# Kernel optimization log

Hardware: AMD Instinct MI355X
Metric: run time of the kernel (lower is better)

## Reference

```python
import jax, jax.numpy as jnp
import numpy as np

N_NODES = 100000
N_EDGES = 1600000
IN_DIM, FEAT_DIM, HID_DIM, OUT_DIM = 128, 64, 64, 64


def _linear_params(key, fan_in, fan_out):
    kw, kb = jax.random.split(key)
    bound = 1.0 / np.sqrt(fan_in)
    W = jax.random.uniform(kw, (fan_out, fan_in), jnp.float32, -bound, bound)
    b = jax.random.uniform(kb, (fan_out,), jnp.float32, -bound, bound)
    return W, b


def setup_inputs() -> dict:
    key = jax.random.key(0)
    k_x, k1, k2, k3, k_e = jax.random.split(key, 5)
    x = jax.random.normal(k_x, (N_NODES, IN_DIM), jnp.float32)
    edge_index = jax.random.randint(k_e, (2, N_EDGES), 0, N_NODES, jnp.int32)
    W_pre, b_pre = _linear_params(k1, IN_DIM, FEAT_DIM)
    W_first, b_first = _linear_params(k2, FEAT_DIM, HID_DIM)
    W_out, b_out = _linear_params(k3, HID_DIM, OUT_DIM)
    return {"x": x, "edge_index": edge_index,
            "W_pre": W_pre, "b_pre": b_pre,
            "W_first": W_first, "b_first": b_first,
            "W_out": W_out, "b_out": b_out}


def _gin_conv(x, src, dst, W, b):
    # out_i = nn((1+eps)*x_i + sum_{j: (j->i)} x_j), eps=0 (PyG GINConv default)
    msgs = x[src]                                   # [E, d] gather
    agg = jax.ops.segment_sum(msgs, dst, num_segments=x.shape[0])  # [N, d]
    return (x + agg) @ W.T + b


def reference(x, edge_index, W_pre, b_pre, W_first, b_first, W_out, b_out):
    src, dst = edge_index[0], edge_index[1]
    h = x @ W_pre.T + b_pre                         # feature_pre linear
    h = _gin_conv(h, src, dst, W_first, b_first)
    h = jax.nn.relu(h)                              # dropout: eval mode no-op
    h = _gin_conv(h, src, dst, W_out, b_out)
    return h
```

## Files before the change

kernel.cpp:

```cpp
#include <hip/hip_runtime.h>


using bf16x8 = __attribute__((ext_vector_type(8))) short;
using f32x4  = __attribute__((ext_vector_type(4))) float;

__device__ inline unsigned short f2bf(float f) {
    unsigned b = __float_as_uint(f);
    return (unsigned short)((b + 0x7FFF + ((b >> 16) & 1)) >> 16);
}
__device__ inline float bf2f_lo(unsigned u) { return __uint_as_float(u << 16); }
__device__ inline float bf2f_hi(unsigned u) { return __uint_as_float(u & 0xFFFF0000u); }
__device__ inline unsigned packbf(float lo, float hi) {
    return (unsigned)f2bf(lo) | ((unsigned)f2bf(hi) << 16);
}
__device__ inline void acc8(float* a, const uint4 u) {
    a[0] += bf2f_lo(u.x); a[1] += bf2f_hi(u.x);
    a[2] += bf2f_lo(u.y); a[3] += bf2f_hi(u.y);
    a[4] += bf2f_lo(u.z); a[5] += bf2f_hi(u.z);
    a[6] += bf2f_lo(u.w); a[7] += bf2f_hi(u.w);
}

constexpr int CHUNK = 4096;
constexpr int LCAP  = 1024;

__global__ __launch_bounds__(256) void k1_pre_hist(
    const float* __restrict__ x, const float* __restrict__ Wp,
    const float* __restrict__ bp, unsigned short* __restrict__ h16a, int N,
    const int* __restrict__ dst, int* __restrict__ ccounts,
    int E, int NBKC, int NC, int GB)
{
    __shared__ char lds_raw[34816];
    const int tid = threadIdx.x;

    if (blockIdx.x >= GB) {
        int* cnt = (int*)lds_raw;
        const int c = blockIdx.x - GB;
        for (int b = tid; b < NBKC; b += 256) cnt[b] = 0;
        __syncthreads();
        const int beg = c * CHUNK, end = min(beg + CHUNK, E);
        for (int e = beg + tid; e < end; e += 256)
            atomicAdd(&cnt[dst[e] >> 8], 1);
        __syncthreads();
        for (int b = tid; b < NBKC; b += 256) ccounts[b * NC + c] = cnt[b];
        return;
    }

    constexpr int SP = 136;
    unsigned short (*xs)[SP] = (unsigned short(*)[SP])lds_raw;
    unsigned short (*ws)[SP] = (unsigned short(*)[SP])(lds_raw + 64 * SP * 2);
    const int base = blockIdx.x * 64;

    for (int i = tid; i < 64 * 32; i += 256) {
        const int r = i >> 5, q = i & 31;
        const float4 v = *(const float4*)(Wp + r * 128 + q * 4);
        *(ushort4*)&ws[r][q * 4] =
            make_ushort4(f2bf(v.x), f2bf(v.y), f2bf(v.z), f2bf(v.w));
    }
    for (int i = tid; i < 64 * 32; i += 256) {
        const int r = i >> 5, q = i & 31;
        int row = base + r; if (row > N - 1) row = N - 1;
        const float4 v = *(const float4*)(x + (size_t)row * 128 + q * 4);
        *(ushort4*)&xs[r][q * 4] =
            make_ushort4(f2bf(v.x), f2bf(v.y), f2bf(v.z), f2bf(v.w));
    }
    __syncthreads();

    const int w = tid >> 6, l = tid & 63, lr = l & 15, lg = l >> 4;
    f32x4 acc[4];
#pragma unroll
    for (int nb = 0; nb < 4; ++nb) {
        const float bv = bp[nb * 16 + lr];
        acc[nb] = (f32x4){bv, bv, bv, bv};
    }
#pragma unroll
    for (int kb = 0; kb < 4; ++kb) {
        const bf16x8 a = *(const bf16x8*)&xs[w * 16 + lr][kb * 32 + lg * 8];
#pragma unroll
        for (int nb = 0; nb < 4; ++nb) {
            const bf16x8 b = *(const bf16x8*)&ws[nb * 16 + lr][kb * 32 + lg * 8];
            acc[nb] = __builtin_amdgcn_mfma_f32_16x16x32_bf16(a, b, acc[nb], 0, 0, 0);
        }
    }
#pragma unroll
    for (int nb = 0; nb < 4; ++nb) {
#pragma unroll
        for (int r = 0; r < 4; ++r) {
            const int row = base + w * 16 + lg * 4 + r;
            if (row < N)
                h16a[(size_t)row * 64 + nb * 16 + lr] = f2bf(acc[nb][r]);
        }
    }
}

__global__ __launch_bounds__(512) void k_blocksum(
    const int* __restrict__ in, int* __restrict__ partial, int n)
{
    __shared__ int s[512];
    const int i = blockIdx.x * 512 + threadIdx.x;
    s[threadIdx.x] = (i < n) ? in[i] : 0;
    __syncthreads();
    for (int off = 256; off > 0; off >>= 1) {
        if (threadIdx.x < off) s[threadIdx.x] += s[threadIdx.x + off];
        __syncthreads();
    }
    if (threadIdx.x == 0) partial[blockIdx.x] = s[0];
}

__global__ __launch_bounds__(1024) void k_scanpartial1024(
    int* __restrict__ partial, int nblk)
{
    __shared__ int s[1024];
    const int t = threadIdx.x;
    s[t] = (t < nblk) ? partial[t] : 0;
    __syncthreads();
    for (int off = 1; off < 1024; off <<= 1) {
        const int v = (t >= off) ? s[t - off] : 0;
        __syncthreads();
        s[t] += v;
        __syncthreads();
    }
    if (t < nblk) partial[t] = (t == 0) ? 0 : s[t - 1];
}

__global__ __launch_bounds__(512) void k_exscan(
    int* __restrict__ data, const int* __restrict__ partial, int n)
{
    __shared__ int s[512];
    const int i = blockIdx.x * 512 + threadIdx.x;
    const int t = threadIdx.x;
    const int v = (i < n) ? data[i] : 0;
    s[t] = v;
    __syncthreads();
    for (int off = 1; off < 512; off <<= 1) {
        const int u = (t >= off) ? s[t - off] : 0;
        __syncthreads();
        s[t] += u;
        __syncthreads();
    }
    if (i < n) data[i] = partial[blockIdx.x] + s[t] - v;
}

__global__ __launch_bounds__(256) void p_coarse(
    const int* __restrict__ src, const int* __restrict__ dst,
    const int* __restrict__ ccounts, unsigned* __restrict__ slots,
    int E, int NBKC, int NC)
{
    __shared__ int cur[512];
    const int c = blockIdx.x;
    for (int b = threadIdx.x; b < NBKC; b += 256) cur[b] = ccounts[b * NC + c];
    __syncthreads();
    const int beg = c * CHUNK;
    const int end = min(beg + CHUNK, E);
    for (int e = beg + threadIdx.x; e < end; e += 256) {
        const int d = dst[e];
        const int pos = atomicAdd(&cur[d >> 8], 1);
        slots[pos] = ((unsigned)(d & 255) << 24) | (unsigned)src[e];
    }
}

__global__ __launch_bounds__(256) void p_fine(
    const unsigned* __restrict__ slots, const int* __restrict__ ccounts,
    unsigned* __restrict__ slots2, int* __restrict__ noffs,
    int E, int N, int NBKC, int NC)
{
    __shared__ int hist[256], psum[256], cur[256];
    const int cb  = blockIdx.x;
    const int tid = threadIdx.x;
    const int cbase = ccounts[cb * NC];
    const int cend  = (cb + 1 < NBKC) ? ccounts[(cb + 1) * NC] : E;

    hist[tid] = 0;
    __syncthreads();
    for (int i = cbase + tid; i < cend; i += 256)
        atomicAdd(&hist[slots[i] >> 24], 1);
    __syncthreads();

    psum[tid] = hist[tid];
    __syncthreads();
    for (int off = 1; off < 256; off <<= 1) {
        const int v = (tid >= off) ? psum[tid - off] : 0;
        __syncthreads();
        psum[tid] += v;
        __syncthreads();
    }
    const int o = cbase + psum[tid] - hist[tid];
    cur[tid] = o;
    const int gnode = cb * 256 + tid;
    if (gnode < N) noffs[gnode] = o;
    if (cb == NBKC - 1 && tid == 0) noffs[N] = cend;
    __syncthreads();

    for (int i = cbase + tid; i < cend; i += 256) {
        const unsigned p = slots[i];
        const int pos = atomicAdd(&cur[p >> 24], 1);
        slots2[pos] = p & 0x00FFFFFFu;
    }
}

template <int RELU, int WF32>
__global__ __launch_bounds__(128) void conv_fused(
    const unsigned short* __restrict__ hin, const unsigned* __restrict__ slots2,
    const int* __restrict__ noffs, const float* __restrict__ W,
    const float* __restrict__ bias, float* __restrict__ outf,
    unsigned short* __restrict__ out16, int N)
{
    constexpr int SPW = 72;
    __shared__ unsigned short ws[64][SPW];
    __shared__ unsigned short xs[32][SPW];
    __shared__ unsigned lsl[LCAP];
    __shared__ int loffs[33];
    __shared__ int steal;

    const int tid  = threadIdx.x;
    const int base = blockIdx.x * 32;

    for (int i = tid; i < 64 * 16; i += 128) {
        const int r = i >> 4, q = i & 15;
        const float4 v = *(const float4*)(W + r * 64 + q * 4);
        *(ushort4*)&ws[r][q * 4] =
            make_ushort4(f2bf(v.x), f2bf(v.y), f2bf(v.z), f2bf(v.w));
    }
    if (tid <= 32) loffs[tid] = noffs[min(base + tid, N)];
    if (tid == 0) steal = 0;
    __syncthreads();

    const int beg = loffs[0];
    const int cnt = loffs[32] - beg;
    for (int i = tid; i < min(cnt, LCAP); i += 128) lsl[i] = slots2[beg + i];
    __syncthreads();

    const int l = tid & 63;
    const int leader = l & ~7;
    const int c = (l & 7) * 8;
    while (true) {
        int n = 0;
        if ((l & 7) == 0) n = atomicAdd(&steal, 1);
        n = __shfl(n, leader);
        if (n >= 32) break;
        const int node = base + n;
        float a[8] = {0.f, 0.f, 0.f, 0.f, 0.f, 0.f, 0.f, 0.f};
        if (node < N) {
            acc8(a, *(const uint4*)(hin + (size_t)node * 64 + c));
            int j = loffs[n] - beg;
            const int hi = loffs[n + 1] - beg;
            const int hiL = min(hi, LCAP);
            for (; j + 8 <= hiL; j += 8) {
                const unsigned s0 = lsl[j],     s1 = lsl[j + 1];
                const unsigned s2 = lsl[j + 2], s3 = lsl[j + 3];
                const unsigned s4 = lsl[j + 4], s5 = lsl[j + 5];
                const unsigned s6 = lsl[j + 6], s7 = lsl[j + 7];
                const uint4 u0 = *(const uint4*)(hin + (size_t)s0 * 64 + c);
                const uint4 u1 = *(const uint4*)(hin + (size_t)s1 * 64 + c);
                const uint4 u2 = *(const uint4*)(hin + (size_t)s2 * 64 + c);
                const uint4 u3 = *(const uint4*)(hin + (size_t)s3 * 64 + c);
                const uint4 u4 = *(const uint4*)(hin + (size_t)s4 * 64 + c);
                const uint4 u5 = *(const uint4*)(hin + (size_t)s5 * 64 + c);
                const uint4 u6 = *(const uint4*)(hin + (size_t)s6 * 64 + c);
                const uint4 u7 = *(const uint4*)(hin + (size_t)s7 * 64 + c);
                acc8(a, u0); acc8(a, u1); acc8(a, u2); acc8(a, u3);
                acc8(a, u4); acc8(a, u5); acc8(a, u6); acc8(a, u7);
            }
            for (; j + 4 <= hiL; j += 4) {
                const unsigned s0 = lsl[j],     s1 = lsl[j + 1];
                const unsigned s2 = lsl[j + 2], s3 = lsl[j + 3];
                const uint4 u0 = *(const uint4*)(hin + (size_t)s0 * 64 + c);
                const uint4 u1 = *(const uint4*)(hin + (size_t)s1 * 64 + c);
                const uint4 u2 = *(const uint4*)(hin + (size_t)s2 * 64 + c);
                const uint4 u3 = *(const uint4*)(hin + (size_t)s3 * 64 + c);
                acc8(a, u0); acc8(a, u1); acc8(a, u2); acc8(a, u3);
            }
            for (; j < hiL; ++j)
                acc8(a, *(const uint4*)(hin + (size_t)lsl[j] * 64 + c));
            for (; j < hi; ++j) {
                const unsigned s = slots2[beg + j];
                acc8(a, *(const uint4*)(hin + (size_t)s * 64 + c));
            }
        }
        *(uint4*)&xs[n][c] =
            make_uint4(packbf(a[0], a[1]), packbf(a[2], a[3]),
                       packbf(a[4], a[5]), packbf(a[6], a[7]));
    }
    __syncthreads();

    const int w = tid >> 6, lr = l & 15, lg = l >> 4;
    f32x4 acc[4];
#pragma unroll
    for (int nb = 0; nb < 4; ++nb) {
        const float bv = bias[nb * 16 + lr];
        acc[nb] = (f32x4){bv, bv, bv, bv};
    }
#pragma unroll
    for (int kb = 0; kb < 2; ++kb) {
        const bf16x8 a = *(const bf16x8*)&xs[w * 16 + lr][kb * 32 + lg * 8];
#pragma unroll
        for (int nb = 0; nb < 4; ++nb) {
            const bf16x8 b = *(const bf16x8*)&ws[nb * 16 + lr][kb * 32 + lg * 8];
            acc[nb] = __builtin_amdgcn_mfma_f32_16x16x32_bf16(a, b, acc[nb], 0, 0, 0);
        }
    }
#pragma unroll
    for (int nb = 0; nb < 4; ++nb) {
#pragma unroll
        for (int r = 0; r < 4; ++r) {
            const int row = base + w * 16 + lg * 4 + r;
            if (row < N) {
                float v = acc[nb][r];
                if (RELU) v = fmaxf(v, 0.f);
                if (WF32) outf[(size_t)row * 64 + nb * 16 + lr] = v;
                else      out16[(size_t)row * 64 + nb * 16 + lr] = f2bf(v);
            }
        }
    }
}

extern "C" void kernel_launch(void* const* d_in, const int* in_sizes, int n_in,
                              void* d_out, int out_size, void* d_ws, size_t ws_size,
                              hipStream_t stream)
{
    const float* x       = (const float*)d_in[0];
    const int*   ei      = (const int*)  d_in[1];
    const float* W_pre   = (const float*)d_in[2];
    const float* b_pre   = (const float*)d_in[3];
    const float* W_first = (const float*)d_in[4];
    const float* b_first = (const float*)d_in[5];
    const float* W_out   = (const float*)d_in[6];
    const float* b_out   = (const float*)d_in[7];

    const int N = in_sizes[0] / 128;
    const int E = in_sizes[1] / 2;
    const int* src = ei;
    const int* dst = ei + E;

    const int NBKC  = (N + 255) / 256;
    const int NC    = (E + CHUNK - 1) / CHUNK;
    const int nscan = NBKC * NC;
    const int nsblk = (nscan + 511) / 512;
    const int GB    = (N + 63) / 64;
    const int CB    = (N + 31) / 32;

    unsigned short* h16a   = (unsigned short*)d_ws;
    unsigned short* h16b   = h16a + (size_t)N * 64;
    unsigned*       slots  = (unsigned*)(h16b + (size_t)N * 64);
    unsigned*       slots2 = slots + E;
    int*            ccounts= (int*)(slots2 + E);
    int*            partial= ccounts + nscan;
    int*            noffs  = partial + 1024;

    float* out = (float*)d_out;

    k1_pre_hist<<<GB + NC, 256, 0, stream>>>(
        x, W_pre, b_pre, h16a, N, dst, ccounts, E, NBKC, NC, GB);

    k_blocksum<<<nsblk, 512, 0, stream>>>(ccounts, partial, nscan);
    k_scanpartial1024<<<1, 1024, 0, stream>>>(partial, nsblk);
    k_exscan<<<nsblk, 512, 0, stream>>>(ccounts, partial, nscan);

    p_coarse<<<NC, 256, 0, stream>>>(src, dst, ccounts, slots, E, NBKC, NC);
    p_fine<<<NBKC, 256, 0, stream>>>(slots, ccounts, slots2, noffs, E, N, NBKC, NC);

    conv_fused<1, 0><<<CB, 128, 0, stream>>>(
        h16a, slots2, noffs, W_first, b_first, nullptr, h16b, N);

    conv_fused<0, 1><<<CB, 128, 0, stream>>>(
        h16b, slots2, noffs, W_out, b_out, out, nullptr, N);
}
```

Measured before the change: 139.4 us.

## Split pre-GEMM across coarse/fine partition kernels and load W fragments into registers

Moves the input linear layer tiles out of the histogram kernel and splits them in half, running each half as extra blocks of the coarse-scatter and fine-sort kernels. This fills the small, latency-bound partition launches with independent compute work. The conv kernel also drops its LDS weight staging and loads the bf16 weight fragments straight from global memory into registers, reading noffs directly. The cost is more register pressure and larger LDS use in the sort kernels, which share a binary with the GEMM path.

```diff
diff --git a/kernel.cpp b/kernel.cpp
--- a/kernel.cpp
+++ b/kernel.cpp
@@ -23,32 +23,14 @@
 constexpr int CHUNK = 4096;
 constexpr int LCAP  = 1024;
 
-__global__ __launch_bounds__(256) void k1_pre_hist(
-    const float* __restrict__ x, const float* __restrict__ Wp,
-    const float* __restrict__ bp, unsigned short* __restrict__ h16a, int N,
-    const int* __restrict__ dst, int* __restrict__ ccounts,
-    int E, int NBKC, int NC, int GB)
-{
-    __shared__ char lds_raw[34816];
+__device__ __forceinline__ void pre_gemm_tile(
+    int base, const float* __restrict__ x, const float* __restrict__ Wp,
+    const float* __restrict__ bp, unsigned short* __restrict__ h16a, int N)
+{
+    constexpr int SP = 136;
+    __shared__ unsigned short xs[64][SP];
+    __shared__ unsigned short ws[64][SP];
     const int tid = threadIdx.x;
-
-    if (blockIdx.x >= GB) {
-        int* cnt = (int*)lds_raw;
-        const int c = blockIdx.x - GB;
-        for (int b = tid; b < NBKC; b += 256) cnt[b] = 0;
-        __syncthreads();
-        const int beg = c * CHUNK, end = min(beg + CHUNK, E);
-        for (int e = beg + tid; e < end; e += 256)
-            atomicAdd(&cnt[dst[e] >> 8], 1);
-        __syncthreads();
-        for (int b = tid; b < NBKC; b += 256) ccounts[b * NC + c] = cnt[b];
-        return;
-    }
-
-    constexpr int SP = 136;
-    unsigned short (*xs)[SP] = (unsigned short(*)[SP])lds_raw;
-    unsigned short (*ws)[SP] = (unsigned short(*)[SP])(lds_raw + 64 * SP * 2);
-    const int base = blockIdx.x * 64;
 
     for (int i = tid; i < 64 * 32; i += 256) {
         const int r = i >> 5, q = i & 31;
@@ -92,6 +74,22 @@
     }
 }
 
+__global__ __launch_bounds__(256) void p_hist(
+    const int* __restrict__ dst, int* __restrict__ ccounts,
+    int E, int NBKC, int NC)
+{
+    __shared__ int cnt[512];
+    const int tid = threadIdx.x;
+    const int c = blockIdx.x;
+    for (int b = tid; b < NBKC; b += 256) cnt[b] = 0;
+    __syncthreads();
+    const int beg = c * CHUNK, end = min(beg + CHUNK, E);
+    for (int e = beg + tid; e < end; e += 256)
+        atomicAdd(&cnt[dst[e] >> 8], 1);
+    __syncthreads();
+    for (int b = tid; b < NBKC; b += 256) ccounts[b * NC + c] = cnt[b];
+}
+
 __global__ __launch_bounds__(512) void k_blocksum(
     const int* __restrict__ in, int* __restrict__ partial, int n)
 {
@@ -140,61 +138,73 @@
     if (i < n) data[i] = partial[blockIdx.x] + s[t] - v;
 }
 
-__global__ __launch_bounds__(256) void p_coarse(
+__global__ __launch_bounds__(256) void k_coarse_gemm(
     const int* __restrict__ src, const int* __restrict__ dst,
     const int* __restrict__ ccounts, unsigned* __restrict__ slots,
-    int E, int NBKC, int NC)
-{
-    __shared__ int cur[512];
-    const int c = blockIdx.x;
-    for (int b = threadIdx.x; b < NBKC; b += 256) cur[b] = ccounts[b * NC + c];
-    __syncthreads();
-    const int beg = c * CHUNK;
-    const int end = min(beg + CHUNK, E);
-    for (int e = beg + threadIdx.x; e < end; e += 256) {
-        const int d = dst[e];
-        const int pos = atomicAdd(&cur[d >> 8], 1);
-        slots[pos] = ((unsigned)(d & 255) << 24) | (unsigned)src[e];
-    }
-}
-
-__global__ __launch_bounds__(256) void p_fine(
+    const float* __restrict__ x, const float* __restrict__ Wp,
+    const float* __restrict__ bp, unsigned short* __restrict__ h16a,
+    int N, int E, int NBKC, int NC)
+{
+    if ((int)blockIdx.x < NC) {
+        __shared__ int cur[512];
+        const int c = blockIdx.x;
+        for (int b = threadIdx.x; b < NBKC; b += 256) cur[b] = ccounts[b * NC + c];
+        __syncthreads();
+        const int beg = c * CHUNK;
+        const int end = min(beg + CHUNK, E);
+        for (int e = beg + threadIdx.x; e < end; e += 256) {
+            const int d = dst[e];
+            const int pos = atomicAdd(&cur[d >> 8], 1);
+            slots[pos] = ((unsigned)(d & 255) << 24) | (unsigned)src[e];
+        }
+        return;
+    }
+    pre_gemm_tile((blockIdx.x - NC) * 64, x, Wp, bp, h16a, N);
+}
+
+__global__ __launch_bounds__(256) void k_fine_gemm(
     const unsigned* __restrict__ slots, const int* __restrict__ ccounts,
     unsigned* __restrict__ slots2, int* __restrict__ noffs,
-    int E, int N, int NBKC, int NC)
-{
-    __shared__ int hist[256], psum[256], cur[256];
-    const int cb  = blockIdx.x;
-    const int tid = threadIdx.x;
-    const int cbase = ccounts[cb * NC];
-    const int cend  = (cb + 1 < NBKC) ? ccounts[(cb + 1) * NC] : E;
-
-    hist[tid] = 0;
-    __syncthreads();
-    for (int i = cbase + tid; i < cend; i += 256)
-        atomicAdd(&hist[slots[i] >> 24], 1);
-    __syncthreads();
-
-    psum[tid] = hist[tid];
-    __syncthreads();
-    for (int off = 1; off < 256; off <<= 1) {
-        const int v = (tid >= off) ? psum[tid - off] : 0;
-        __syncthreads();
-        psum[tid] += v;
-        __syncthreads();
-    }
-    const int o = cbase + psum[tid] - hist[tid];
-    cur[tid] = o;
-    const int gnode = cb * 256 + tid;
-    if (gnode < N) noffs[gnode] = o;
-    if (cb == NBKC - 1 && tid == 0) noffs[N] = cend;
-    __syncthreads();
-
-    for (int i = cbase + tid; i < cend; i += 256) {
-        const unsigned p = slots[i];
-        const int pos = atomicAdd(&cur[p >> 24], 1);
-        slots2[pos] = p & 0x00FFFFFFu;
-    }
+    const float* __restrict__ x, const float* __restrict__ Wp,
+    const float* __restrict__ bp, unsigned short* __restrict__ h16a,
+    int GA, int N, int E, int NBKC, int NC)
+{
+    if ((int)blockIdx.x < NBKC) {
+        __shared__ int hist[256], psum[256], cur[256];
+        const int cb  = blockIdx.x;
+        const int tid = threadIdx.x;
+        const int cbase = ccounts[cb * NC];
+        const int cend  = (cb + 1 < NBKC) ? ccounts[(cb + 1) * NC] : E;
+
+        hist[tid] = 0;
+        __syncthreads();
+        for (int i = cbase + tid; i < cend; i += 256)
+            atomicAdd(&hist[slots[i] >> 24], 1);
+        __syncthreads();
+
+        psum[tid] = hist[tid];
+        __syncthreads();
+        for (int off = 1; off < 256; off <<= 1) {
+            const int v = (tid >= off) ? psum[tid - off] : 0;
+            __syncthreads();
+            psum[tid] += v;
+            __syncthreads();
+        }
+        const int o = cbase + psum[tid] - hist[tid];
+        cur[tid] = o;
+        const int gnode = cb * 256 + tid;
+        if (gnode < N) noffs[gnode] = o;
+        if (cb == NBKC - 1 && tid == 0) noffs[N] = cend;
+        __syncthreads();
+
+        for (int i = cbase + tid; i < cend; i += 256) {
+            const unsigned p = slots[i];
+            const int pos = atomicAdd(&cur[p >> 24], 1);
+            slots2[pos] = p & 0x00FFFFFFu;
+        }
+        return;
+    }
+    pre_gemm_tile((GA + blockIdx.x - NBKC) * 64, x, Wp, bp, h16a, N);
 }
 
 template <int RELU, int WF32>
@@ -205,7 +215,6 @@
     unsigned short* __restrict__ out16, int N)
 {
     constexpr int SPW = 72;
-    __shared__ unsigned short ws[64][SPW];
     __shared__ unsigned short xs[32][SPW];
     __shared__ unsigned lsl[LCAP];
     __shared__ int loffs[33];
@@ -214,18 +223,11 @@
     const int tid  = threadIdx.x;
     const int base = blockIdx.x * 32;
 
-    for (int i = tid; i < 64 * 16; i += 128) {
-        const int r = i >> 4, q = i & 15;
-        const float4 v = *(const float4*)(W + r * 64 + q * 4);
-        *(ushort4*)&ws[r][q * 4] =
-            make_ushort4(f2bf(v.x), f2bf(v.y), f2bf(v.z), f2bf(v.w));
-    }
     if (tid <= 32) loffs[tid] = noffs[min(base + tid, N)];
     if (tid == 0) steal = 0;
-    __syncthreads();
-
-    const int beg = loffs[0];
-    const int cnt = loffs[32] - beg;
+    const int beg  = noffs[base];
+    const int cend = noffs[min(base + 32, N)];
+    const int cnt  = cend - beg;
     for (int i = tid; i < min(cnt, LCAP); i += 128) lsl[i] = slots2[beg + i];
     __syncthreads();
 
@@ -283,6 +285,23 @@
     __syncthreads();
 
     const int w = tid >> 6, lr = l & 15, lg = l >> 4;
+    bf16x8 wf[2][4];
+#pragma unroll
+    for (int kb = 0; kb < 2; ++kb) {
+#pragma unroll
+        for (int nb = 0; nb < 4; ++nb) {
+            const float* wp = W + (nb * 16 + lr) * 64 + kb * 32 + lg * 8;
+            const float4 v0 = *(const float4*)wp;
+            const float4 v1 = *(const float4*)(wp + 4);
+            bf16x8 b;
+            b[0] = (short)f2bf(v0.x); b[1] = (short)f2bf(v0.y);
+            b[2] = (short)f2bf(v0.z); b[3] = (short)f2bf(v0.w);
+            b[4] = (short)f2bf(v1.x); b[5] = (short)f2bf(v1.y);
+            b[6] = (short)f2bf(v1.z); b[7] = (short)f2bf(v1.w);
+            wf[kb][nb] = b;
+        }
+    }
+
     f32x4 acc[4];
 #pragma unroll
     for (int nb = 0; nb < 4; ++nb) {
@@ -294,8 +313,7 @@
         const bf16x8 a = *(const bf16x8*)&xs[w * 16 + lr][kb * 32 + lg * 8];
 #pragma unroll
         for (int nb = 0; nb < 4; ++nb) {
-            const bf16x8 b = *(const bf16x8*)&ws[nb * 16 + lr][kb * 32 + lg * 8];
-            acc[nb] = __builtin_amdgcn_mfma_f32_16x16x32_bf16(a, b, acc[nb], 0, 0, 0);
+            acc[nb] = __builtin_amdgcn_mfma_f32_16x16x32_bf16(a, wf[kb][nb], acc[nb], 0, 0, 0);
         }
     }
 #pragma unroll
@@ -336,6 +354,7 @@
     const int nscan = NBKC * NC;
     const int nsblk = (nscan + 511) / 512;
     const int GB    = (N + 63) / 64;
+    const int GA    = GB / 2;
     const int CB    = (N + 31) / 32;
 
     unsigned short* h16a   = (unsigned short*)d_ws;
@@ -348,15 +367,18 @@
 
     float* out = (float*)d_out;
 
-    k1_pre_hist<<<GB + NC, 256, 0, stream>>>(
-        x, W_pre, b_pre, h16a, N, dst, ccounts, E, NBKC, NC, GB);
+    p_hist<<<NC, 256, 0, stream>>>(dst, ccounts, E, NBKC, NC);
 
     k_blocksum<<<nsblk, 512, 0, stream>>>(ccounts, partial, nscan);
     k_scanpartial1024<<<1, 1024, 0, stream>>>(partial, nsblk);
     k_exscan<<<nsblk, 512, 0, stream>>>(ccounts, partial, nscan);
 
-    p_coarse<<<NC, 256, 0, stream>>>(src, dst, ccounts, slots, E, NBKC, NC);
-    p_fine<<<NBKC, 256, 0, stream>>>(slots, ccounts, slots2, noffs, E, N, NBKC, NC);
+    k_coarse_gemm<<<NC + GA, 256, 0, stream>>>(
+        src, dst, ccounts, slots, x, W_pre, b_pre, h16a, N, E, NBKC, NC);
+
+    k_fine_gemm<<<NBKC + (GB - GA), 256, 0, stream>>>(
+        slots, ccounts, slots2, noffs, x, W_pre, b_pre, h16a,
+        GA, N, E, NBKC, NC);
 
     conv_fused<1, 0><<<CB, 128, 0, stream>>>(
         h16a, slots2, noffs, W_first, b_first, nullptr, h16b, N);
```

After: 146.1 us. 4.8% more time.
